# Optimization experiments

Hardware: AMD Instinct MI355X
Metric: run time of the kernel (lower is better)

Reference implementation:

```python
import jax, jax.numpy as jnp
import numpy as np


def _wn(v, g):
    # weight norm over input axis: w[:, j] = g[j] * v[:, j] / ||v[:, j]||
    norm = jnp.sqrt(jnp.sum(v * v, axis=0, keepdims=True))
    return v * (g[None, :] / norm)


def setup_inputs() -> dict:
    key = jax.random.key(0)
    ks = jax.random.split(key, 6)
    M, K1, H, OUT = 65536, 512, 1024, 512
    x = jax.random.normal(ks[0], (M, K1), dtype=jnp.float32)
    v1 = jax.random.normal(ks[1], (K1, H), dtype=jnp.float32) * 0.05
    v2 = jax.random.normal(ks[2], (H, H), dtype=jnp.float32) * 0.05
    v3 = jax.random.normal(ks[3], (H, H), dtype=jnp.float32) * 0.05
    v4 = jax.random.normal(ks[4], (H, H), dtype=jnp.float32) * 0.05
    v5 = jax.random.normal(ks[5], (H, OUT), dtype=jnp.float32) * 0.05
    g1 = jnp.ones((H,), jnp.float32)
    g2 = jnp.ones((H,), jnp.float32)
    g3 = jnp.ones((H,), jnp.float32)
    g4 = jnp.ones((H,), jnp.float32)
    g5 = jnp.ones((OUT,), jnp.float32)
    return {"x": x, "v1": v1, "g1": g1, "v2": v2, "g2": g2,
            "v3": v3, "g3": g3, "v4": v4, "g4": g4, "v5": v5, "g5": g5}


def reference(x, v1, g1, v2, g2, v3, g3, v4, g4, v5, g5):
    w1 = _wn(v1, g1)
    w2 = _wn(v2, g2)
    w3 = _wn(v3, g3)
    w4 = _wn(v4, g4)
    w5 = _wn(v5, g5)
    h1 = jax.nn.softplus(x @ w1)    # [M, H]
    h2 = jax.nn.softplus(h1 @ w2)
    h3 = jax.nn.softplus(h2 @ w3)
    h4 = jax.nn.softplus(h3 @ w4)
    out = h4 @ w5                   # final layer linear
    return out
```

## Files before the change

### kernel.cpp

```cpp
#include <hip/hip_runtime.h>
#include <hip/hip_bf16.h>
#include <cstdint>

typedef unsigned short u16;
typedef __attribute__((ext_vector_type(8))) _Float16 f16x8;
typedef __attribute__((ext_vector_type(4))) float f32x4;
typedef __attribute__((ext_vector_type(8))) unsigned short u16x8;

typedef const __attribute__((address_space(1))) void* gas1p;
typedef __attribute__((address_space(3))) void* las3p;

__device__ __forceinline__ void gld_lds16(const void* g, void* l) {
    __builtin_amdgcn_global_load_lds((gas1p)g, (las3p)l, 16, 0, 0);
}

__device__ __forceinline__ u16 f2h(float f) {
    _Float16 h = (_Float16)f;
    return __builtin_bit_cast(u16, h);
}

__global__ void cvt_x_kernel(const float4* __restrict__ x, u16* __restrict__ xb) {
    size_t i = (size_t)blockIdx.x * blockDim.x + threadIdx.x;
    float4 a = x[2 * i];
    float4 b = x[2 * i + 1];
    u16x8 o;
    o[0] = f2h(a.x); o[1] = f2h(a.y); o[2] = f2h(a.z); o[3] = f2h(a.w);
    o[4] = f2h(b.x); o[5] = f2h(b.y); o[6] = f2h(b.z); o[7] = f2h(b.w);
    *(u16x8*)&xb[i * 8] = o;
}

__global__ void wn_partial(const float* __restrict__ v, float* __restrict__ partial,
                           int K, int N) {
    int lane = threadIdx.x & 63;
    int tr = threadIdx.x >> 6;
    int n = blockIdx.x * 64 + lane;
    int kseg = K >> 3;
    int kbeg = blockIdx.y * kseg;
    float s = 0.f;
    for (int k = kbeg + tr; k < kbeg + kseg; k += 4) {
        float x = v[(size_t)k * N + n];
        s += x * x;
    }
    __shared__ float red[4][64];
    red[tr][lane] = s;
    __syncthreads();
    if (tr == 0)
        partial[blockIdx.y * N + n] = red[0][lane] + red[1][lane] + red[2][lane] + red[3][lane];
}

__global__ void wn_scale(const float* __restrict__ partial, const float* __restrict__ g,
                         float* __restrict__ scale, int N) {
    int n = blockIdx.x * 256 + threadIdx.x;
    if (n < N) {
        float s = 0.f;
        for (int i = 0; i < 8; i++) s += partial[i * N + n];
        scale[n] = g[n] / sqrtf(s);
    }
}

__global__ void wn_write(const float* __restrict__ v, const float* __restrict__ scale,
                         u16* __restrict__ wT, int K, int N) {
    int lane = threadIdx.x & 63;
    int tr = threadIdx.x >> 6;
    int n = blockIdx.x * 64 + lane;
    int kseg = K >> 3;
    int kbeg = blockIdx.y * kseg;
    float sc = scale[n];
    for (int k = kbeg + tr; k < kbeg + kseg; k += 4)
        wT[(size_t)n * K + k] = f2h(v[(size_t)k * N + n] * sc);
}

template<int N, int K, bool ACT, bool OUTF32>
__global__ __launch_bounds__(512, 2) void gemm_mlp(
    const u16* __restrict__ A, const u16* __restrict__ Bt,
    u16* __restrict__ Ch, float* __restrict__ Cf)
{
    constexpr int M = 65536;
    constexpr int NT = K / 64;
    constexpr int NTN = N / 256;
    constexpr int NWG = (M / 256) * NTN;

    __shared__ u16 sA[2][256 * 64];
    __shared__ u16 sB[2][2 * 128 * 64];

    const int bid = blockIdx.x;
    const int wk = (bid & 7) * (NWG >> 3) + (bid >> 3);
    const int tm = wk / NTN, tn = wk % NTN;
    const long m0 = (long)tm * 256;
    const int n0 = tn * 256;

    const int tid = threadIdx.x;
    const int lane = tid & 63;
    const int wid = tid >> 6;
    const int wm = (wid >> 2) * 128;
    const int wn = (wid & 3) * 64;

    const int r8 = tid >> 3;
    const int gcol = ((tid & 7) ^ (r8 & 7)) * 8;
    const u16* Abase = A + (m0 + r8) * (size_t)K + gcol;
    const u16* Bbase = Bt + (size_t)(n0 + ((r8 >> 5) * 64 + (r8 & 31))) * K + gcol;
    const int dst8 = tid * 8;

    auto stageA = [&](int buf, int t, int q) {
        gld_lds16(Abase + (size_t)q * (64 * (size_t)K) + (size_t)t * 64,
                  &sA[buf][q * 4096 + dst8]);
    };
    auto stageB = [&](int buf, int t, int s, int c) {
        gld_lds16(Bbase + (size_t)(s * 32 + c * 128) * K + (size_t)t * 64,
                  &sB[buf][s * 8192 + c * 4096 + dst8]);
    };

    const int rbase = lane & 15;
    const int co0 = ((lane >> 4) ^ (lane & 7)) * 8;
    const int arow0 = (wm + rbase) * 64 + co0;
    const int brow0 = ((wn >> 6) * 32 + rbase) * 64 + co0;

    f32x4 acc[8][4] = {};
    f16x8 a[4][2], bq[2][2][2];

    auto ldA = [&](int buf, int qm) {
#pragma unroll
        for (int i = 0; i < 4; i++) {
            int base = arow0 + (qm * 64 + i * 16) * 64;
            a[i][0] = *(const f16x8*)&sA[buf][base];
            a[i][1] = *(const f16x8*)&sA[buf][base ^ 32];
        }
    };
    auto ldB = [&](int buf, int qn) {
#pragma unroll
        for (int j2 = 0; j2 < 2; j2++) {
            int base = brow0 + qn * 8192 + j2 * 1024;
            bq[qn][j2][0] = *(const f16x8*)&sB[buf][base];
            bq[qn][j2][1] = *(const f16x8*)&sB[buf][base ^ 32];
        }
    };
    auto mmaq = [&](int qm, int qn) {
        __builtin_amdgcn_s_setprio(1);
#pragma unroll
        for (int i = 0; i < 4; i++)
#pragma unroll
            for (int j2 = 0; j2 < 2; j2++) {
                f32x4 c = acc[qm * 4 + i][qn * 2 + j2];
                c = __builtin_amdgcn_mfma_f32_16x16x32_f16(a[i][0], bq[qn][j2][0], c, 0, 0, 0);
                c = __builtin_amdgcn_mfma_f32_16x16x32_f16(a[i][1], bq[qn][j2][1], c, 0, 0, 0);
                acc[qm * 4 + i][qn * 2 + j2] = c;
            }
        __builtin_amdgcn_s_setprio(0);
    };
    auto bar = [&]() {
        __builtin_amdgcn_sched_barrier(0);
        asm volatile("" ::: "memory");
        __builtin_amdgcn_s_barrier();
        asm volatile("" ::: "memory");
        __builtin_amdgcn_sched_barrier(0);
    };

    stageA(0, 0, 0); stageA(0, 0, 2);
    stageA(0, 0, 1); stageA(0, 0, 3);
    stageB(0, 0, 0, 0); stageB(0, 0, 0, 1);
    stageA(1, 1, 0); stageA(1, 1, 2);
    stageB(0, 0, 1, 0); stageB(0, 0, 1, 1);
    asm volatile("s_waitcnt vmcnt(4)" ::: "memory");
    bar();

#pragma unroll 2
    for (int t = 0; t < NT - 2; t++) {
        const int cur = t & 1, nxt = cur ^ 1;
        stageA(nxt, t + 1, 1); stageA(nxt, t + 1, 3);
        ldA(cur, 0); ldB(cur, 0);
        asm volatile("s_waitcnt vmcnt(2)" ::: "memory");
        bar();
        mmaq(0, 0);
        stageB(nxt, t + 1, 0, 0); stageB(nxt, t + 1, 0, 1);
        ldB(cur, 1);
        bar();
        mmaq(0, 1);
        stageA(cur, t + 2, 0); stageA(cur, t + 2, 2);
        ldA(cur, 1);
        bar();
        mmaq(1, 0);
        stageB(nxt, t + 1, 1, 0); stageB(nxt, t + 1, 1, 1);
        asm volatile("s_waitcnt vmcnt(4)" ::: "memory");
        bar();
        mmaq(1, 1);
    }
    {
        const int t = NT - 2, cur = t & 1, nxt = cur ^ 1;
        stageA(nxt, t + 1, 1); stageA(nxt, t + 1, 3);
        ldA(cur, 0); ldB(cur, 0);
        asm volatile("s_waitcnt vmcnt(2)" ::: "memory");
        bar();
        mmaq(0, 0);
        stageB(nxt, t + 1, 0, 0); stageB(nxt, t + 1, 0, 1);
        ldB(cur, 1);
        bar();
        mmaq(0, 1);
        ldA(cur, 1);
        bar();
        mmaq(1, 0);
        stageB(nxt, t + 1, 1, 0); stageB(nxt, t + 1, 1, 1);
        asm volatile("s_waitcnt vmcnt(2)" ::: "memory");
        bar();
        mmaq(1, 1);
    }
    {
        const int cur = (NT - 1) & 1;
        ldA(cur, 0); ldB(cur, 0);
        asm volatile("s_waitcnt vmcnt(0)" ::: "memory");
        bar();
        mmaq(0, 0);
        ldB(cur, 1);
        bar();
        mmaq(0, 1);
        ldA(cur, 1);
        bar();
        mmaq(1, 0);
        bar();
        mmaq(1, 1);
    }

    const long crow0 = m0 + wm + ((lane >> 4) << 2);
    const int ccol0 = n0 + wn + (lane & 15);
#pragma unroll
    for (int fi = 0; fi < 8; fi++) {
#pragma unroll
        for (int r = 0; r < 4; r++) {
            const size_t rowoff = (size_t)(crow0 + fi * 16 + r) * N;
#pragma unroll
            for (int fj = 0; fj < 4; fj++) {
                float v = acc[fi][fj][r];
                if (ACT) v = fmaxf(v, 0.f) + __logf(1.f + __expf(-fabsf(v)));
                if (OUTF32) Cf[rowoff + ccol0 + fj * 16] = v;
                else        Ch[rowoff + ccol0 + fj * 16] = f2h(v);
            }
        }
    }
}

extern "C" void kernel_launch(void* const* d_in, const int* in_sizes, int n_in,
                              void* d_out, int out_size, void* d_ws, size_t ws_size,
                              hipStream_t stream) {
    const float* x  = (const float*)d_in[0];
    const float* v1 = (const float*)d_in[1];
    const float* g1 = (const float*)d_in[2];
    const float* v2 = (const float*)d_in[3];
    const float* g2 = (const float*)d_in[4];
    const float* v3 = (const float*)d_in[5];
    const float* g3 = (const float*)d_in[6];
    const float* v4 = (const float*)d_in[7];
    const float* g4 = (const float*)d_in[8];
    const float* v5 = (const float*)d_in[9];
    const float* g5 = (const float*)d_in[10];
    float* out = (float*)d_out;

    const int M = 65536;
    char* ws = (char*)d_ws;
    u16* bufA = (u16*)(ws);
    u16* bufB = (u16*)(ws + 0x8000000ULL);
    u16* w1T  = (u16*)(ws + 0x10000000ULL);
    u16* w2T  = w1T + 1024 * 512;
    u16* w3T  = w2T + 1024 * 1024;
    u16* w4T  = w3T + 1024 * 1024;
    u16* w5T  = w4T + 1024 * 1024;
    float* partial = (float*)(ws + 0x10800000ULL);
    float* scale   = partial + 8 * 1024;

    cvt_x_kernel<<<(M * 512) / (256 * 8), 256, 0, stream>>>((const float4*)x, bufB);

    auto prep = [&](const float* v, const float* g, u16* wT, int K, int N) {
        wn_partial<<<dim3(N / 64, 8), 256, 0, stream>>>(v, partial, K, N);
        wn_scale<<<(N + 255) / 256, 256, 0, stream>>>(partial, g, scale, N);
        wn_write<<<dim3(N / 64, 8), 256, 0, stream>>>(v, scale, wT, K, N);
    };
    prep(v1, g1, w1T, 512, 1024);
    prep(v2, g2, w2T, 1024, 1024);
    prep(v3, g3, w3T, 1024, 1024);
    prep(v4, g4, w4T, 1024, 1024);
    prep(v5, g5, w5T, 1024, 512);

    gemm_mlp<1024, 512,  true,  false><<<1024, 512, 0, stream>>>(bufB, w1T, bufA, nullptr);
    gemm_mlp<1024, 1024, true,  false><<<1024, 512, 0, stream>>>(bufA, w2T, bufB, nullptr);
    gemm_mlp<1024, 1024, true,  false><<<1024, 512, 0, stream>>>(bufB, w3T, bufA, nullptr);
    gemm_mlp<1024, 1024, true,  false><<<1024, 512, 0, stream>>>(bufA, w4T, bufB, nullptr);
    gemm_mlp<512,  1024, false, true ><<<512,  512, 0, stream>>>(bufB, w5T, nullptr, out);

    (void)in_sizes; (void)n_in; (void)out_size; (void)ws_size;
}
```

Measured before the change: 825.1 us.

## Fuse weight-norm prep kernels and reschedule GEMM load/barrier pipeline

Replaces the three-kernel weight-norm prep with one fused kernel per layer that reduces, computes the scale and writes the transposed fp16 weights. The GEMM main loop is reordered: the B staging is spread across the sub-steps, the vmcnt wait moves to a single point, the epilogue barriers are dropped and sched_barriers are removed. Per-quarter pointers are precomputed and the MFMA loop order is changed so k-halves are interleaved. The fused prep kernel uses far fewer blocks, and the changed wait placement risks races or stalls.

```diff
diff --git a/kernel.cpp b/kernel.cpp
--- a/kernel.cpp
+++ b/kernel.cpp
@@ -29,45 +29,26 @@
     *(u16x8*)&xb[i * 8] = o;
 }
 
-__global__ void wn_partial(const float* __restrict__ v, float* __restrict__ partial,
-                           int K, int N) {
-    int lane = threadIdx.x & 63;
-    int tr = threadIdx.x >> 6;
-    int n = blockIdx.x * 64 + lane;
-    int kseg = K >> 3;
-    int kbeg = blockIdx.y * kseg;
-    float s = 0.f;
-    for (int k = kbeg + tr; k < kbeg + kseg; k += 4) {
-        float x = v[(size_t)k * N + n];
-        s += x * x;
-    }
-    __shared__ float red[4][64];
-    red[tr][lane] = s;
-    __syncthreads();
-    if (tr == 0)
-        partial[blockIdx.y * N + n] = red[0][lane] + red[1][lane] + red[2][lane] + red[3][lane];
-}
-
-__global__ void wn_scale(const float* __restrict__ partial, const float* __restrict__ g,
-                         float* __restrict__ scale, int N) {
-    int n = blockIdx.x * 256 + threadIdx.x;
-    if (n < N) {
-        float s = 0.f;
-        for (int i = 0; i < 8; i++) s += partial[i * N + n];
-        scale[n] = g[n] / sqrtf(s);
-    }
-}
-
-__global__ void wn_write(const float* __restrict__ v, const float* __restrict__ scale,
+__global__ void wn_fused(const float* __restrict__ v, const float* __restrict__ g,
                          u16* __restrict__ wT, int K, int N) {
     int lane = threadIdx.x & 63;
     int tr = threadIdx.x >> 6;
     int n = blockIdx.x * 64 + lane;
-    int kseg = K >> 3;
-    int kbeg = blockIdx.y * kseg;
-    float sc = scale[n];
-    for (int k = kbeg + tr; k < kbeg + kseg; k += 4)
-        wT[(size_t)n * K + k] = f2h(v[(size_t)k * N + n] * sc);
+    float s = 0.f;
+    for (int k = tr; k < K; k += 4) {
+        float x = v[(size_t)k * N + n];
+        s += x * x;
+    }
+    __shared__ float red[4][64];
+    __shared__ float sc[64];
+    red[tr][lane] = s;
+    __syncthreads();
+    if (threadIdx.x < 64)
+        sc[lane] = g[n] / sqrtf(red[0][lane] + red[1][lane] + red[2][lane] + red[3][lane]);
+    __syncthreads();
+    float scale = sc[lane];
+    for (int k = tr; k < K; k += 4)
+        wT[(size_t)n * K + k] = f2h(v[(size_t)k * N + n] * scale);
 }
 
 template<int N, int K, bool ACT, bool OUTF32>
@@ -101,13 +82,20 @@
     const u16* Bbase = Bt + (size_t)(n0 + ((r8 >> 5) * 64 + (r8 & 31))) * K + gcol;
     const int dst8 = tid * 8;
 
-    auto stageA = [&](int buf, int t, int q) {
-        gld_lds16(Abase + (size_t)q * (64 * (size_t)K) + (size_t)t * 64,
-                  &sA[buf][q * 4096 + dst8]);
-    };
-    auto stageB = [&](int buf, int t, int s, int c) {
-        gld_lds16(Bbase + (size_t)(s * 32 + c * 128) * K + (size_t)t * 64,
-                  &sB[buf][s * 8192 + c * 4096 + dst8]);
+    const u16* Aq0 = Abase;
+    const u16* Aq1 = Abase + (size_t)64 * K;
+    const u16* Aq2 = Abase + (size_t)128 * K;
+    const u16* Aq3 = Abase + (size_t)192 * K;
+    const u16* B00 = Bbase;
+    const u16* B01 = Bbase + (size_t)128 * K;
+    const u16* B10 = Bbase + (size_t)32 * K;
+    const u16* B11 = Bbase + (size_t)160 * K;
+
+    auto stA = [&](int buf, const u16* base, int t, int q) {
+        gld_lds16(base + (size_t)t * 64, &sA[buf][q * 4096 + dst8]);
+    };
+    auto stB = [&](int buf, const u16* base, int t, int s, int c) {
+        gld_lds16(base + (size_t)t * 64, &sB[buf][s * 8192 + c * 4096 + dst8]);
     };
 
     const int rbase = lane & 15;
@@ -137,85 +125,75 @@
     auto mmaq = [&](int qm, int qn) {
         __builtin_amdgcn_s_setprio(1);
 #pragma unroll
-        for (int i = 0; i < 4; i++)
-#pragma unroll
-            for (int j2 = 0; j2 < 2; j2++) {
-                f32x4 c = acc[qm * 4 + i][qn * 2 + j2];
-                c = __builtin_amdgcn_mfma_f32_16x16x32_f16(a[i][0], bq[qn][j2][0], c, 0, 0, 0);
-                c = __builtin_amdgcn_mfma_f32_16x16x32_f16(a[i][1], bq[qn][j2][1], c, 0, 0, 0);
-                acc[qm * 4 + i][qn * 2 + j2] = c;
-            }
+        for (int kk = 0; kk < 2; kk++)
+#pragma unroll
+            for (int i = 0; i < 4; i++)
+#pragma unroll
+                for (int j2 = 0; j2 < 2; j2++)
+                    acc[qm * 4 + i][qn * 2 + j2] = __builtin_amdgcn_mfma_f32_16x16x32_f16(
+                        a[i][kk], bq[qn][j2][kk], acc[qm * 4 + i][qn * 2 + j2], 0, 0, 0);
         __builtin_amdgcn_s_setprio(0);
     };
     auto bar = [&]() {
-        __builtin_amdgcn_sched_barrier(0);
         asm volatile("" ::: "memory");
         __builtin_amdgcn_s_barrier();
         asm volatile("" ::: "memory");
-        __builtin_amdgcn_sched_barrier(0);
-    };
-
-    stageA(0, 0, 0); stageA(0, 0, 2);
-    stageA(0, 0, 1); stageA(0, 0, 3);
-    stageB(0, 0, 0, 0); stageB(0, 0, 0, 1);
-    stageA(1, 1, 0); stageA(1, 1, 2);
-    stageB(0, 0, 1, 0); stageB(0, 0, 1, 1);
-    asm volatile("s_waitcnt vmcnt(4)" ::: "memory");
+    };
+
+    stA(0, Aq0, 0, 0); stA(0, Aq2, 0, 2);
+    stB(0, B00, 0, 0, 0); stB(0, B01, 0, 0, 1);
+    stB(0, B10, 0, 1, 0); stB(0, B11, 0, 1, 1);
+    stA(0, Aq1, 0, 1); stA(0, Aq3, 0, 3);
+    stA(1, Aq0, 1, 0); stA(1, Aq2, 1, 2);
+    asm volatile("s_waitcnt vmcnt(2)" ::: "memory");
     bar();
 
 #pragma unroll 2
     for (int t = 0; t < NT - 2; t++) {
         const int cur = t & 1, nxt = cur ^ 1;
-        stageA(nxt, t + 1, 1); stageA(nxt, t + 1, 3);
+        stA(nxt, Aq1, t + 1, 1); stA(nxt, Aq3, t + 1, 3);
         ldA(cur, 0); ldB(cur, 0);
+        bar();
+        mmaq(0, 0);
+        stB(nxt, B00, t + 1, 0, 0); stB(nxt, B01, t + 1, 0, 1);
+        ldB(cur, 1);
+        bar();
+        mmaq(0, 1);
+        stB(nxt, B10, t + 1, 1, 0); stB(nxt, B11, t + 1, 1, 1);
+        ldA(cur, 1);
+        bar();
+        mmaq(1, 0);
+        stA(cur, Aq0, t + 2, 0); stA(cur, Aq2, t + 2, 2);
         asm volatile("s_waitcnt vmcnt(2)" ::: "memory");
-        bar();
-        mmaq(0, 0);
-        stageB(nxt, t + 1, 0, 0); stageB(nxt, t + 1, 0, 1);
-        ldB(cur, 1);
-        bar();
-        mmaq(0, 1);
-        stageA(cur, t + 2, 0); stageA(cur, t + 2, 2);
-        ldA(cur, 1);
-        bar();
-        mmaq(1, 0);
-        stageB(nxt, t + 1, 1, 0); stageB(nxt, t + 1, 1, 1);
-        asm volatile("s_waitcnt vmcnt(4)" ::: "memory");
         bar();
         mmaq(1, 1);
     }
     {
         const int t = NT - 2, cur = t & 1, nxt = cur ^ 1;
-        stageA(nxt, t + 1, 1); stageA(nxt, t + 1, 3);
+        stA(nxt, Aq1, t + 1, 1); stA(nxt, Aq3, t + 1, 3);
         ldA(cur, 0); ldB(cur, 0);
-        asm volatile("s_waitcnt vmcnt(2)" ::: "memory");
         bar();
         mmaq(0, 0);
-        stageB(nxt, t + 1, 0, 0); stageB(nxt, t + 1, 0, 1);
+        stB(nxt, B00, t + 1, 0, 0); stB(nxt, B01, t + 1, 0, 1);
         ldB(cur, 1);
         bar();
         mmaq(0, 1);
+        stB(nxt, B10, t + 1, 1, 0); stB(nxt, B11, t + 1, 1, 1);
         ldA(cur, 1);
         bar();
         mmaq(1, 0);
-        stageB(nxt, t + 1, 1, 0); stageB(nxt, t + 1, 1, 1);
-        asm volatile("s_waitcnt vmcnt(2)" ::: "memory");
+        asm volatile("s_waitcnt vmcnt(0)" ::: "memory");
         bar();
         mmaq(1, 1);
     }
     {
         const int cur = (NT - 1) & 1;
         ldA(cur, 0); ldB(cur, 0);
-        asm volatile("s_waitcnt vmcnt(0)" ::: "memory");
-        bar();
         mmaq(0, 0);
         ldB(cur, 1);
-        bar();
         mmaq(0, 1);
         ldA(cur, 1);
-        bar();
         mmaq(1, 0);
-        bar();
         mmaq(1, 1);
     }
 
@@ -262,21 +240,14 @@
     u16* w3T  = w2T + 1024 * 1024;
     u16* w4T  = w3T + 1024 * 1024;
     u16* w5T  = w4T + 1024 * 1024;
-    float* partial = (float*)(ws + 0x10800000ULL);
-    float* scale   = partial + 8 * 1024;
 
     cvt_x_kernel<<<(M * 512) / (256 * 8), 256, 0, stream>>>((const float4*)x, bufB);
 
-    auto prep = [&](const float* v, const float* g, u16* wT, int K, int N) {
-        wn_partial<<<dim3(N / 64, 8), 256, 0, stream>>>(v, partial, K, N);
-        wn_scale<<<(N + 255) / 256, 256, 0, stream>>>(partial, g, scale, N);
-        wn_write<<<dim3(N / 64, 8), 256, 0, stream>>>(v, scale, wT, K, N);
-    };
-    prep(v1, g1, w1T, 512, 1024);
-    prep(v2, g2, w2T, 1024, 1024);
-    prep(v3, g3, w3T, 1024, 1024);
-    prep(v4, g4, w4T, 1024, 1024);
-    prep(v5, g5, w5T, 1024, 512);
+    wn_fused<<<1024 / 64, 256, 0, stream>>>(v1, g1, w1T, 512, 1024);
+    wn_fused<<<1024 / 64, 256, 0, stream>>>(v2, g2, w2T, 1024, 1024);
+    wn_fused<<<1024 / 64, 256, 0, stream>>>(v3, g3, w3T, 1024, 1024);
+    wn_fused<<<1024 / 64, 256, 0, stream>>>(v4, g4, w4T, 1024, 1024);
+    wn_fused<<<512 / 64, 256, 0, stream>>>(v5, g5, w5T, 1024, 512);
 
     gemm_mlp<1024, 512,  true,  false><<<1024, 512, 0, stream>>>(bufB, w1T, bufA, nullptr);
     gemm_mlp<1024, 1024, true,  false><<<1024, 512, 0, stream>>>(bufA, w2T, bufB, nullptr);
```

After: 1.384 ms. 1.68x slower.
